# Performance work log

Hardware: AMD Instinct MI355X
Metric: run time of the kernel (lower is better)

The kernel has to match this reference:

```python
import jax, jax.numpy as jnp
import numpy as np

B, C, H, W = 4, 512, 64, 208
HID = 512          # params.text_hidden_dim; must equal C for view(1,C,H,-1)
DS = 16            # 1/scale_factor for nearest downsample of the mask
N_REG = 4          # four region-indexed attention modules


def setup_inputs() -> dict:
    key = jax.random.key(0)
    ks = jax.random.split(key, 7)
    image_feature = jax.random.normal(ks[0], (B, C, H, W), dtype=jnp.float32)
    text_feat = jax.random.normal(ks[1], (N_REG, B, HID), dtype=jnp.float32)
    # Mask is constant per (full-res) column so that each region's pixel count
    # is divisible by H, as the original view(1, C, H, -1) requires.
    col_labels = jax.random.randint(ks[2], (B, W * DS), 1, N_REG + 1)
    text_mask = jnp.broadcast_to(
        col_labels[:, None, None, :], (B, 1, H * DS, W * DS)
    ).astype(jnp.int32)
    # Per-region MHA params (nn.Linear weights, no bias assumed).
    Wq = jax.random.normal(ks[3], (N_REG, C, HID), dtype=jnp.float32) * (C ** -0.5)
    Wk = jax.random.normal(ks[4], (N_REG, HID, HID), dtype=jnp.float32) * (HID ** -0.5)
    Wv = jax.random.normal(ks[5], (N_REG, HID, HID), dtype=jnp.float32) * (HID ** -0.5)
    Wo = jax.random.normal(ks[6], (N_REG, HID, C), dtype=jnp.float32) * (HID ** -0.5)
    return {
        "image_feature": image_feature,
        "text_feat": text_feat,
        "text_mask": text_mask,
        "Wq": Wq,
        "Wk": Wk,
        "Wv": Wv,
        "Wo": Wo,
    }


def reference(image_feature, text_feat, text_mask, Wq, Wk, Wv, Wo):
    # F.interpolate(scale=1/16, mode='nearest') == strided slicing for integer stride.
    mask_ds = text_mask[:, 0, ::DS, ::DS]          # [B, H, W]
    col_labels = mask_ds[:, 0, :]                  # [B, W] (mask is column-constant)
    # Cross-attention of every region pixel (query) against ONE text token z
    # (single key/value): softmax over a length-1 axis is identically 1, so
    # attn_out = Wo @ (Wv @ z) for every pixel, and Wq/Wk receive zero gradient.
    # With the residual connection: out_pixel = x_pixel + (z Wv) Wo per region.
    delta = jnp.einsum('rbh,rhd,rdc->brc', text_feat, Wv, Wo)          # [B, R, C]
    d_col = jnp.take_along_axis(delta, (col_labels - 1)[:, :, None], axis=1)  # [B, W, C]
    out = image_feature + d_col.transpose(0, 2, 1)[:, :, None, :]      # [B, C, H, W]
    # The torch code concatenates regions along width in sorted-unique label
    # order, i.e. columns are permuted by (label, original column) -- a stable
    # argsort of the column labels.
    order = jnp.argsort(col_labels, axis=1, stable=True)               # [B, W]
    return jnp.take_along_axis(out, order[:, None, None, :], axis=3)
```

## Files before the change

### kernel.cpp

```cpp
#include <hip/hip_runtime.h>

#define B_ 4
#define C_ 512
#define H_ 64
#define W_ 208
#define HID_ 512
#define NREG_ 4
#define DS_ 16


__global__ __launch_bounds__(256) void prepA_kernel(
    const float* __restrict__ tf, const float* __restrict__ Wv,
    const int* __restrict__ mask, float* __restrict__ tmp, int* __restrict__ swl) {
  int blk = blockIdx.x, tid = threadIdx.x;
  if (blk < 256) {
    int r = blk >> 6;
    int h0 = ((blk >> 3) & 7) * 64;
    int d0 = (blk & 7) * 64;
    int g = tid >> 6, dd = tid & 63;
    __shared__ float tf_s[B_][64];
    __shared__ float red[4][B_][64];
    tf_s[g][dd] = tf[(r * B_ + g) * HID_ + h0 + dd];
    __syncthreads();
    float acc[B_] = {};
    for (int hh = g * 16; hh < g * 16 + 16; ++hh) {
      float w = Wv[(size_t)(r * HID_ + h0 + hh) * HID_ + d0 + dd];
#pragma unroll
      for (int b = 0; b < B_; ++b) acc[b] += tf_s[b][hh] * w;
    }
#pragma unroll
    for (int b = 0; b < B_; ++b) red[g][b][dd] = acc[b];
    __syncthreads();
    {
      float s = red[0][g][dd] + red[1][g][dd] + red[2][g][dd] + red[3][g][dd];
      atomicAdd(&tmp[(g * NREG_ + r) * HID_ + d0 + dd], s);
    }
  } else {
    int b = blk - 256;
    const size_t mb = (size_t)b * (H_ * DS_) * (W_ * DS_);
    int w = tid;
    int l = (w < W_) ? (mask[mb + (size_t)w * DS_] - 1) : -1;
    int wave = tid >> 6, lane = tid & 63;
    unsigned long long bal[NREG_];
    __shared__ int wcnt[4][NREG_];
#pragma unroll
    for (int r = 0; r < NREG_; ++r) bal[r] = __ballot(l == r);
    if (lane < NREG_) wcnt[wave][lane] = __popcll(bal[lane]);
    __syncthreads();
    if (w < W_) {
      int pos = 0;
#pragma unroll
      for (int q = 0; q < NREG_; ++q) {
        int tot = wcnt[0][q] + wcnt[1][q] + wcnt[2][q] + wcnt[3][q];
        if (q < l) pos += tot;
      }
#pragma unroll
      for (int v = 0; v < 4; ++v)
        if (v < wave) pos += wcnt[v][l];
      pos += __popcll(bal[l] & ((1ull << lane) - 1ull));
      swl[b * W_ + pos] = w | (l << 16);
    }
  }
}

__global__ __launch_bounds__(256) void prepB_kernel(
    const float* __restrict__ tmp, const float* __restrict__ Wo,
    float* __restrict__ delta) {
  int blk = blockIdx.x, tid = threadIdx.x;
  int r = blk >> 6;
  int d0 = ((blk >> 3) & 7) * 64;
  int c0 = (blk & 7) * 64;
  int g = tid >> 6, cc = tid & 63;
  __shared__ float tmp_s[B_][64];
  __shared__ float red[4][B_][64];
  tmp_s[g][cc] = tmp[(g * NREG_ + r) * HID_ + d0 + cc];
  __syncthreads();
  float acc[B_] = {};
  for (int dd = g * 16; dd < g * 16 + 16; ++dd) {
    float w = Wo[(size_t)(r * HID_ + d0 + dd) * C_ + c0 + cc];
#pragma unroll
    for (int b = 0; b < B_; ++b) acc[b] += tmp_s[b][dd] * w;
  }
#pragma unroll
  for (int b = 0; b < B_; ++b) red[g][b][cc] = acc[b];
  __syncthreads();
  {
    float s = red[0][g][cc] + red[1][g][cc] + red[2][g][cc] + red[3][g][cc];
    atomicAdd(&delta[(g * NREG_ + r) * C_ + c0 + cc], s);
  }
}

#define RCH_ (W_ / 4)
#define TROWS_ 16
#define TF4_ (TROWS_ * RCH_)
__global__ __launch_bounds__(256, 8) void apply_kernel(
    const float* __restrict__ img, const float* __restrict__ delta,
    const int* __restrict__ swl, float* __restrict__ out) {
  int blk = blockIdx.x;
  int b = blk >> 9;
  int tid = threadIdx.x;
  __shared__ int swl_s[W_];
  __shared__ float dval[W_];
  __shared__ float dsel_s[NREG_];
  __shared__ float tile[TROWS_ * W_];
  if (tid < W_) swl_s[tid] = swl[b * W_ + tid];
  if (tid < NREG_) dsel_s[tid] = delta[(b * NREG_ + tid) * C_ + (blk & (C_ - 1))];
  __syncthreads();
  if (tid < W_) {
    int e = swl_s[tid];
    dval[e & 0xFFFF] = dsel_s[e >> 16];
  }
  __syncthreads();
  const float4* srcv = (const float4*)(img + (size_t)blk * (H_ * W_));
  float4* dstv = (float4*)(out + (size_t)blk * (H_ * W_));
  const float4* dval4 = (const float4*)dval;
  const int4* swl4 = (const int4*)swl_s;
  for (int t = 0; t < H_ / TROWS_; ++t) {
    int base = t * TF4_;
#pragma unroll
    for (int g = 0; g < 4; ++g) {
      int ii = g * 256 + tid;
      if (ii < TF4_) {
        float4 v = srcv[base + ii];
        int hl = ii / RCH_;
        int j = ii - hl * RCH_;
        float4 dv = dval4[j];
        float4 o;
        o.x = v.x + dv.x; o.y = v.y + dv.y; o.z = v.z + dv.z; o.w = v.w + dv.w;
        ((float4*)&tile[hl * W_])[j] = o;
      }
    }
    __syncthreads();
#pragma unroll
    for (int g = 0; g < 4; ++g) {
      int ii = g * 256 + tid;
      if (ii < TF4_) {
        int hl = ii / RCH_;
        int jo = ii - hl * RCH_;
        int4 sw = swl4[jo];
        const float* rowp = &tile[hl * W_];
        float4 o;
        o.x = rowp[sw.x & 0xFFFF];
        o.y = rowp[sw.y & 0xFFFF];
        o.z = rowp[sw.z & 0xFFFF];
        o.w = rowp[sw.w & 0xFFFF];
        dstv[base + ii] = o;
      }
    }
    __syncthreads();
  }
}

extern "C" void kernel_launch(void* const* d_in, const int* in_sizes, int n_in,
                              void* d_out, int out_size, void* d_ws, size_t ws_size,
                              hipStream_t stream) {
  const float* img  = (const float*)d_in[0];
  const float* tf   = (const float*)d_in[1];
  const int*   mask = (const int*)d_in[2];
  const float* Wv   = (const float*)d_in[5];
  const float* Wo   = (const float*)d_in[6];
  float* delta = (float*)d_ws;
  float* tmp   = (float*)((char*)d_ws + 32768);
  int*   swl   = (int*)((char*)d_ws + 65536);
  float* out   = (float*)d_out;

  hipMemsetAsync(d_ws, 0, 65536, stream);
  prepA_kernel<<<260, 256, 0, stream>>>(tf, Wv, mask, tmp, swl);
  prepB_kernel<<<256, 256, 0, stream>>>(tmp, Wo, delta);
  apply_kernel<<<B_ * C_, 256, 0, stream>>>(img, delta, swl, out);
}
```

Before: 245.3 us.

## Fuse Wo projection into apply kernel, drop memset and atomics, prefetch image tiles

Removes the memset and the separate prepB kernel by having each apply block compute its own four delta values (a dot of tmp with one Wo column) via wave shuffle reduction. prepA now has each block reduce over the full hidden dimension, so it writes tmp directly instead of using atomics, with fewer and longer-running blocks. The apply kernel also prefetches the next image tile into registers while the current tile is permuted. The trade-off is strided, uncoalesced Wo column reads repeated for every batch index, extra register pressure, and much less parallelism in the Wv stage.

```diff
diff --git a/kernel.cpp b/kernel.cpp
--- a/kernel.cpp
+++ b/kernel.cpp
@@ -9,34 +9,38 @@
 #define DS_ 16
 
 
-__global__ __launch_bounds__(256) void prepA_kernel(
+__global__ __launch_bounds__(256) void prep_kernel(
     const float* __restrict__ tf, const float* __restrict__ Wv,
     const int* __restrict__ mask, float* __restrict__ tmp, int* __restrict__ swl) {
   int blk = blockIdx.x, tid = threadIdx.x;
-  if (blk < 256) {
-    int r = blk >> 6;
-    int h0 = ((blk >> 3) & 7) * 64;
+  if (blk < 32) {
+    int r = blk >> 3;
     int d0 = (blk & 7) * 64;
     int g = tid >> 6, dd = tid & 63;
-    __shared__ float tf_s[B_][64];
+    __shared__ float tf_s[B_ * HID_];
     __shared__ float red[4][B_][64];
-    tf_s[g][dd] = tf[(r * B_ + g) * HID_ + h0 + dd];
+#pragma unroll
+    for (int k = 0; k < 8; ++k) {
+      int idx = k * 256 + tid;
+      tf_s[idx] = tf[r * (B_ * HID_) + idx];
+    }
     __syncthreads();
     float acc[B_] = {};
-    for (int hh = g * 16; hh < g * 16 + 16; ++hh) {
-      float w = Wv[(size_t)(r * HID_ + h0 + hh) * HID_ + d0 + dd];
+#pragma unroll 4
+    for (int hh = g * 128; hh < g * 128 + 128; ++hh) {
+      float w = Wv[(size_t)(r * HID_ + hh) * HID_ + d0 + dd];
 #pragma unroll
-      for (int b = 0; b < B_; ++b) acc[b] += tf_s[b][hh] * w;
+      for (int b = 0; b < B_; ++b) acc[b] += tf_s[b * HID_ + hh] * w;
     }
 #pragma unroll
     for (int b = 0; b < B_; ++b) red[g][b][dd] = acc[b];
     __syncthreads();
     {
       float s = red[0][g][dd] + red[1][g][dd] + red[2][g][dd] + red[3][g][dd];
-      atomicAdd(&tmp[(g * NREG_ + r) * HID_ + d0 + dd], s);
+      tmp[(g * NREG_ + r) * HID_ + d0 + dd] = s;
     }
   } else {
-    int b = blk - 256;
+    int b = blk - 32;
     const size_t mb = (size_t)b * (H_ * DS_) * (W_ * DS_);
     int w = tid;
     int l = (w < W_) ? (mask[mb + (size_t)w * DS_] - 1) : -1;
@@ -63,67 +67,72 @@
   }
 }
 
-__global__ __launch_bounds__(256) void prepB_kernel(
-    const float* __restrict__ tmp, const float* __restrict__ Wo,
-    float* __restrict__ delta) {
-  int blk = blockIdx.x, tid = threadIdx.x;
-  int r = blk >> 6;
-  int d0 = ((blk >> 3) & 7) * 64;
-  int c0 = (blk & 7) * 64;
-  int g = tid >> 6, cc = tid & 63;
-  __shared__ float tmp_s[B_][64];
-  __shared__ float red[4][B_][64];
-  tmp_s[g][cc] = tmp[(g * NREG_ + r) * HID_ + d0 + cc];
-  __syncthreads();
-  float acc[B_] = {};
-  for (int dd = g * 16; dd < g * 16 + 16; ++dd) {
-    float w = Wo[(size_t)(r * HID_ + d0 + dd) * C_ + c0 + cc];
-#pragma unroll
-    for (int b = 0; b < B_; ++b) acc[b] += tmp_s[b][dd] * w;
-  }
-#pragma unroll
-  for (int b = 0; b < B_; ++b) red[g][b][cc] = acc[b];
-  __syncthreads();
-  {
-    float s = red[0][g][cc] + red[1][g][cc] + red[2][g][cc] + red[3][g][cc];
-    atomicAdd(&delta[(g * NREG_ + r) * C_ + c0 + cc], s);
-  }
-}
-
 #define RCH_ (W_ / 4)
 #define TROWS_ 16
 #define TF4_ (TROWS_ * RCH_)
+#define NT_ (H_ / TROWS_)
 __global__ __launch_bounds__(256, 8) void apply_kernel(
-    const float* __restrict__ img, const float* __restrict__ delta,
-    const int* __restrict__ swl, float* __restrict__ out) {
+    const float* __restrict__ img, const float* __restrict__ tmp,
+    const float* __restrict__ Wo, const int* __restrict__ swl,
+    float* __restrict__ out) {
   int blk = blockIdx.x;
   int b = blk >> 9;
+  int c = blk & (C_ - 1);
   int tid = threadIdx.x;
   __shared__ int swl_s[W_];
   __shared__ float dval[W_];
   __shared__ float dsel_s[NREG_];
+  __shared__ float wred[4][NREG_];
   __shared__ float tile[TROWS_ * W_];
+
+  const float4* srcv = (const float4*)(img + (size_t)blk * (H_ * W_));
+  float4* dstv = (float4*)(out + (size_t)blk * (H_ * W_));
+
+  float4 pre[4];
+#pragma unroll
+  for (int g = 0; g < 4; ++g) {
+    int ii = g * 256 + tid;
+    if (ii < TF4_) pre[g] = srcv[ii];
+  }
   if (tid < W_) swl_s[tid] = swl[b * W_ + tid];
-  if (tid < NREG_) dsel_s[tid] = delta[(b * NREG_ + tid) * C_ + (blk & (C_ - 1))];
+
+  float acc[NREG_] = {};
+#pragma unroll
+  for (int k = 0; k < 2; ++k) {
+    int d = k * 256 + tid;
+#pragma unroll
+    for (int r = 0; r < NREG_; ++r)
+      acc[r] += tmp[(b * NREG_ + r) * HID_ + d] * Wo[(size_t)(r * HID_ + d) * C_ + c];
+  }
+#pragma unroll
+  for (int r = 0; r < NREG_; ++r)
+#pragma unroll
+    for (int off = 32; off; off >>= 1) acc[r] += __shfl_down(acc[r], off);
+  int wave = tid >> 6, lane = tid & 63;
+  if (lane == 0) {
+#pragma unroll
+    for (int r = 0; r < NREG_; ++r) wred[wave][r] = acc[r];
+  }
+  __syncthreads();
+  if (tid < NREG_)
+    dsel_s[tid] = wred[0][tid] + wred[1][tid] + wred[2][tid] + wred[3][tid];
   __syncthreads();
   if (tid < W_) {
     int e = swl_s[tid];
     dval[e & 0xFFFF] = dsel_s[e >> 16];
   }
   __syncthreads();
-  const float4* srcv = (const float4*)(img + (size_t)blk * (H_ * W_));
-  float4* dstv = (float4*)(out + (size_t)blk * (H_ * W_));
+
   const float4* dval4 = (const float4*)dval;
   const int4* swl4 = (const int4*)swl_s;
-  for (int t = 0; t < H_ / TROWS_; ++t) {
-    int base = t * TF4_;
+  for (int t = 0; t < NT_; ++t) {
 #pragma unroll
     for (int g = 0; g < 4; ++g) {
       int ii = g * 256 + tid;
       if (ii < TF4_) {
-        float4 v = srcv[base + ii];
         int hl = ii / RCH_;
         int j = ii - hl * RCH_;
+        float4 v = pre[g];
         float4 dv = dval4[j];
         float4 o;
         o.x = v.x + dv.x; o.y = v.y + dv.y; o.z = v.z + dv.z; o.w = v.w + dv.w;
@@ -131,6 +140,13 @@
       }
     }
     __syncthreads();
+    if (t + 1 < NT_) {
+#pragma unroll
+      for (int g = 0; g < 4; ++g) {
+        int ii = g * 256 + tid;
+        if (ii < TF4_) pre[g] = srcv[(t + 1) * TF4_ + ii];
+      }
+    }
 #pragma unroll
     for (int g = 0; g < 4; ++g) {
       int ii = g * 256 + tid;
@@ -144,7 +160,7 @@
         o.y = rowp[sw.y & 0xFFFF];
         o.z = rowp[sw.z & 0xFFFF];
         o.w = rowp[sw.w & 0xFFFF];
-        dstv[base + ii] = o;
+        dstv[t * TF4_ + ii] = o;
       }
     }
     __syncthreads();
@@ -159,13 +175,10 @@
   const int*   mask = (const int*)d_in[2];
   const float* Wv   = (const float*)d_in[5];
   const float* Wo   = (const float*)d_in[6];
-  float* delta = (float*)d_ws;
-  float* tmp   = (float*)((char*)d_ws + 32768);
-  int*   swl   = (int*)((char*)d_ws + 65536);
-  float* out   = (float*)d_out;
+  float* tmp = (float*)d_ws;
+  int*   swl = (int*)((char*)d_ws + 32768);
+  float* out = (float*)d_out;
 
-  hipMemsetAsync(d_ws, 0, 65536, stream);
-  prepA_kernel<<<260, 256, 0, stream>>>(tf, Wv, mask, tmp, swl);
-  prepB_kernel<<<256, 256, 0, stream>>>(tmp, Wo, delta);
-  apply_kernel<<<B_ * C_, 256, 0, stream>>>(img, delta, swl, out);
+  prep_kernel<<<36, 256, 0, stream>>>(tf, Wv, mask, tmp, swl);
+  apply_kernel<<<B_ * C_, 256, 0, stream>>>(img, tmp, Wo, swl, out);
 }
```

Measured after the change: 278.6 us. 13.5% more time.
